# Kernel tuning notes

Hardware: AMD Instinct MI355X
Metric: run time of the kernel (lower is better)

The kernel has to match this reference:

```python
import jax, jax.numpy as jnp
import numpy as np

B, DIM, IN_DIM, H, W = 4, 256, 128, 128, 128
DD = IN_DIM // 2          # down_dim = 64
HEADS = 8
BN_EPS = 1e-5


def conv2d(x, w, b=None, pad=0, dil=1):
    y = jax.lax.conv_general_dilated(
        x, w, window_strides=(1, 1),
        padding=[(pad, pad), (pad, pad)],
        rhs_dilation=(dil, dil),
        dimension_numbers=('NCHW', 'OIHW', 'NCHW'))
    if b is not None:
        y = y + b[None, :, None, None]
    return y


def bn_relu(x, s, o):
    # eval-mode BatchNorm2d with running_mean=0, running_var=1
    return jax.nn.relu(x * (s / np.sqrt(1.0 + BN_EPS))[None, :, None, None] + o[None, :, None, None])


def setup_inputs() -> dict:
    ks = iter(jax.random.split(jax.random.key(0), 80))

    def w(shape, sc=0.05):
        return sc * jax.random.normal(next(ks), shape, jnp.float32)

    def s(c):
        return 1.0 + 0.1 * jax.random.normal(next(ks), (c,), jnp.float32)

    def o(c):
        return 0.02 * jax.random.normal(next(ks), (c,), jnp.float32)

    d = {}
    d['x'] = jax.random.normal(next(ks), (B, DIM, H, W), jnp.float32)
    d['w_dc'] = w((IN_DIM, DIM, 3, 3)); d['b_dc'] = w((IN_DIM,)); d['s_dc'] = s(IN_DIM); d['o_dc'] = o(IN_DIM)
    d['w1'] = w((DD, IN_DIM, 1, 1)); d['b1'] = w((DD,)); d['s1'] = s(DD); d['o1'] = o(DD)
    d['w2'] = w((DD, DD, 3, 3)); d['b2'] = w((DD,)); d['s2'] = s(DD); d['o2'] = o(DD)
    d['w3'] = w((DD, DD, 3, 3)); d['b3'] = w((DD,)); d['s3'] = s(DD); d['o3'] = o(DD)
    d['w4'] = w((DD, DD, 3, 3)); d['b4'] = w((DD,)); d['s4'] = s(DD); d['o4'] = o(DD)
    d['w5'] = w((DD, IN_DIM, 1, 1)); d['b5'] = w((DD,)); d['s5'] = s(DD); d['o5'] = o(DD)
    d['temperature'] = jnp.ones((HEADS, 1, 1), jnp.float32)
    d['w_po'] = w((DD, 2 * DD, 1, 1))  # project_out, bias=False
    d['w_wa'] = w((DD // 16, DD, 1, 1)); d['b_wa'] = w((DD // 16,)); d['s_wa'] = s(DD // 16); d['o_wa'] = o(DD // 16)
    d['w_wb'] = w((DD, DD // 16, 1, 1)); d['b_wb'] = w((DD,))
    d['w_f'] = w((DD, 5 * DD, 1, 1)); d['b_f'] = w((DD,)); d['s_f'] = s(DD); d['o_f'] = o(DD)
    d['w_oa'] = w((DD // 2, DD, 3, 3)); d['b_oa'] = w((DD // 2,)); d['s_oa'] = s(DD // 2); d['o_oa'] = o(DD // 2)
    d['w_ob'] = w((1, DD // 2, 1, 1)); d['b_ob'] = w((1,))
    return d


def reference(x, w_dc, b_dc, s_dc, o_dc, w1, b1, s1, o1, w2, b2, s2, o2,
              w3, b3, s3, o3, w4, b4, s4, o4, w5, b5, s5, o5,
              temperature, w_po, w_wa, b_wa, s_wa, o_wa, w_wb, b_wb,
              w_f, b_f, s_f, o_f, w_oa, b_oa, s_oa, o_oa, w_ob, b_ob):

    def branch(c):
        b, ch, h, wd = c.shape
        f = jnp.fft.fft2(c)                                   # [b,ch,h,w] complex64 (q=k=v=tepqkv)
        qkv = f.reshape(b, HEADS, ch // HEADS, h * wd)        # v (unnormalized)
        n = jnp.sqrt(jnp.sum(jnp.square(jnp.abs(qkv)), axis=-1, keepdims=True))
        qn = qkv / jnp.maximum(n, 1e-12)                      # F.normalize(dim=-1); q == k
        attn = jnp.einsum('bhcn,bhdn->bhcd', qn, qn) * temperature
        # custom complex normalization: separate real/imag softmax
        attn = jax.lax.complex(jax.nn.softmax(attn.real, axis=-1),
                               jax.nn.softmax(attn.imag, axis=-1))
        of = jnp.abs(jnp.fft.ifft2(jnp.einsum('bhcd,bhdn->bhcn', attn, qkv)))  # ifft2 over (c, hw)
        of = of.reshape(b, ch, h, wd)
        g = jax.nn.sigmoid(conv2d(bn_relu(conv2d(f.real, w_wa, b_wa), s_wa, o_wa), w_wb, b_wb))
        ol = jnp.abs(jnp.fft.ifft2(g * f))                    # ifft2 over (h, w)
        return conv2d(jnp.concatenate([of, ol], axis=1), w_po) + c

    xd = bn_relu(conv2d(x, w_dc, b_dc, pad=1), s_dc, o_dc)
    c1 = bn_relu(conv2d(xd, w1, b1), s1, o1)
    c2 = bn_relu(conv2d(c1, w2, b2, pad=3, dil=3), s2, o2)
    F2 = branch(c2)
    c3 = bn_relu(conv2d(c1 + F2, w3, b3, pad=5, dil=5), s3, o3)
    F3 = branch(c3)
    c4 = bn_relu(conv2d(c1 + F3, w4, b4, pad=7, dil=7), s4, o4)
    F4 = branch(c4)
    # conv5: global avg pool -> 1x1 conv -> bilinear upsample of a 1x1 map == broadcast
    c5 = bn_relu(conv2d(jnp.mean(xd, axis=(2, 3), keepdims=True), w5, b5), s5, o5)
    c5 = jnp.broadcast_to(c5, (c5.shape[0], c5.shape[1], xd.shape[2], xd.shape[3]))
    fused = bn_relu(conv2d(jnp.concatenate([c1, F2, F3, F4, c5], axis=1), w_f, b_f), s_f, o_f)
    return conv2d(bn_relu(conv2d(fused, w_oa, b_oa, pad=1), s_oa, o_oa), w_ob, b_ob)
```

## Files before the change

kernel.cpp:

```cpp
#include <hip/hip_runtime.h>

#define S 16384
#define PI_F 3.14159265358979f

struct Ptrs { const float* p[43]; };

enum : int {
  O_SBDC=0, O_SB1=256, O_SB2=512, O_SB3=768, O_SB4=1024, O_SB5=1280,
  O_SBWA=1536, O_SBF=1792, O_SBOA=2048,
  O_M=2304, O_C5=2816, O_NRM=3072, O_GRAM=3328, O_ATT2=7424, O_BEFF=11520,
  O_WB=16384,
  O_PART=147456,
  O_H=180224,
  O_WP=442368,
  O_A=524288,
  O_FIN=8912896,
  O_CC=25690112,
  O_DRE=29884416, O_DIMG=34078720,
  O_ERE=38273024, O_EIM=42467328,
  O_G=46661632
};

typedef short bfrag __attribute__((ext_vector_type(8)));
typedef float ffrag __attribute__((ext_vector_type(4)));

__device__ __forceinline__ float bf2f(unsigned short u){
  union { unsigned int i; float f; } v; v.i = ((unsigned int)u) << 16; return v.f;
}
__device__ __forceinline__ unsigned short f2bf(float f){
  unsigned int x = __float_as_uint(f);
  unsigned int r = x + 0x7fffu + ((x >> 16) & 1u);
  return (unsigned short)(r >> 16);
}

__global__ void prep_sb_kernel(Ptrs P, float* ws){
  const float r = rsqrtf(1.0f + 1e-5f);
  int bi=0, si=0, oi=0, C=0, dst=0;
  switch (blockIdx.x){
    case 0: bi=2; si=3; oi=4; C=128; dst=O_SBDC; break;
    case 1: bi=6; si=7; oi=8; C=64; dst=O_SB1; break;
    case 2: bi=10; si=11; oi=12; C=64; dst=O_SB2; break;
    case 3: bi=14; si=15; oi=16; C=64; dst=O_SB3; break;
    case 4: bi=18; si=19; oi=20; C=64; dst=O_SB4; break;
    case 5: bi=22; si=23; oi=24; C=64; dst=O_SB5; break;
    case 6: bi=28; si=29; oi=30; C=4;  dst=O_SBWA; break;
    case 7: bi=34; si=35; oi=36; C=64; dst=O_SBF; break;
    default: bi=38; si=39; oi=40; C=32; dst=O_SBOA; break;
  }
  for (int c = threadIdx.x; c < C; c += 256){
    float bb = P.p[bi][c], ss = P.p[si][c], oo = P.p[oi][c];
    float sc = ss * r;
    ws[dst + c] = sc;
    ws[dst + C + c] = bb * sc + oo;
  }
}

__global__ __launch_bounds__(256) void xpad_kernel(const float* __restrict__ x,
    unsigned short* __restrict__ XT){
  int yy = blockIdx.x, b = blockIdx.y;
  long obase = ((long)(b*130) + yy) * (130L*256);
  int tid = threadIdx.x;
  if (yy == 0 || yy == 129){
    uint4 z; z.x=0; z.y=0; z.z=0; z.w=0;
    for (int i = tid; i < 130*256/8; i += 256)
      *(uint4*)(XT + obase + (long)i*8) = z;
    return;
  }
  __shared__ float LT[64][129];
  int y = yy - 1;
  for (int c0 = 0; c0 < 256; c0 += 64){
    for (int idx = tid; idx < 64*128; idx += 256){
      int ci = idx >> 7, xx = idx & 127;
      LT[ci][xx] = x[((long)(b*256 + c0 + ci)*128 + y)*128 + xx];
    }
    __syncthreads();
    for (int idx = tid; idx < 128*16; idx += 256){
      int xp = idx >> 4, c4 = (idx & 15)*4;
      ushort4 v;
      v.x = f2bf(LT[c4][xp]);   v.y = f2bf(LT[c4+1][xp]);
      v.z = f2bf(LT[c4+2][xp]); v.w = f2bf(LT[c4+3][xp]);
      *(ushort4*)(XT + obase + (long)(xp+1)*256 + c0 + c4) = v;
    }
    __syncthreads();
  }
  if (tid < 64){
    ushort4 z; z.x=0; z.y=0; z.z=0; z.w=0;
    *(ushort4*)(XT + obase + tid*4) = z;
    *(ushort4*)(XT + obase + 129L*256 + tid*4) = z;
  }
}

__global__ void wt_kernel(const float* __restrict__ w, unsigned short* __restrict__ WH,
    unsigned short* __restrict__ WL){
  for (int e = blockIdx.x*256 + threadIdx.x; e < 294912; e += gridDim.x*256){
    int c32 = e & 31, co = (e >> 5) & 127, kc = (e >> 12) & 7, sh = e >> 15;
    int ky = sh / 3, kx = sh - ky*3;
    int ci = kc*32 + c32;
    float v = w[((long)(co*256 + ci)*3 + ky)*3 + kx];
    unsigned short h = f2bf(v);
    WH[e] = h;
    WL[e] = f2bf(v - bf2f(h));
  }
}

__global__ void wtg_kernel(Ptrs P, unsigned short* __restrict__ WB){
  const float* w; int cout; long off;
  switch (blockIdx.y){
    case 0: w = P.p[9];  cout = 64; off = 0;      break;
    case 1: w = P.p[13]; cout = 64; off = 73728;  break;
    case 2: w = P.p[17]; cout = 64; off = 147456; break;
    default: w = P.p[37]; cout = 32; off = 221184; break;
  }
  int total = 576*cout;
  unsigned short* WH = WB + off;
  unsigned short* WL = WH + total;
  for (int e = blockIdx.x*256 + threadIdx.x; e < total; e += gridDim.x*256){
    int c32 = e & 31;
    int co = (e >> 5) & (cout - 1);
    int kc = (e / (32*cout)) & 1;
    int sh = e / (64*cout);
    int ky = sh/3, kx = sh - ky*3;
    int ci = kc*32 + c32;
    float v = w[((long)(co*64 + ci)*3 + ky)*3 + kx];
    unsigned short h = f2bf(v);
    WH[e] = h;
    WL[e] = f2bf(v - bf2f(h));
  }
}

__global__ void wtp_kernel(Ptrs P, unsigned short* __restrict__ WP){
  const float* w; int KC, wstr; long off;
  switch (blockIdx.y){
    case 0: w = P.p[5];  KC = 4; wstr = 128; off = 0;     break;
    case 1: w = P.p[26]; KC = 4; wstr = 128; off = 16384; break;
    default: w = P.p[33]; KC = 8; wstr = 320; off = 32768; break;
  }
  int total = KC*64*32;
  unsigned short* WH = WP + off;
  unsigned short* WL = WH + total;
  for (int e = blockIdx.x*256 + threadIdx.x; e < total; e += gridDim.x*256){
    int c32 = e & 31, co = (e >> 5) & 63, kc = e >> 11;
    float v = w[(long)co*wstr + kc*32 + c32];
    unsigned short h = f2bf(v);
    WH[e] = h;
    WL[e] = f2bf(v - bf2f(h));
  }
}

template<int DIL>
__global__ __launch_bounds__(256) void xpad64_kernel(const float* __restrict__ in1,
    const float* __restrict__ in2, long in_bs, unsigned short* __restrict__ XP){
  constexpr int TW = 128 + 2*DIL;
  int yy = blockIdx.x, b = blockIdx.y;
  long obase = (long)(b*TW + yy) * TW * 64;
  int tid = threadIdx.x;
  if (yy < DIL || yy >= 128 + DIL){
    uint4 z; z.x=0; z.y=0; z.z=0; z.w=0;
    for (int i = tid; i < TW*8; i += 256)
      *(uint4*)(XP + obase + (long)i*8) = z;
    return;
  }
  __shared__ float LT[64][129];
  int y = yy - DIL;
  const float* p1 = in1 + (long)b*in_bs + (long)y*128;
  const float* p2 = in2 ? in2 + (long)b*in_bs + (long)y*128 : nullptr;
  for (int idx = tid; idx < 64*128; idx += 256){
    int ci = idx >> 7, xx = idx & 127;
    float v = p1[(long)ci*S + xx];
    if (p2) v += p2[(long)ci*S + xx];
    LT[ci][xx] = v;
  }
  __syncthreads();
  for (int i = tid; i < 2*DIL*16; i += 256){
    int side = i / (DIL*16);
    int r = i - side*(DIL*16);
    int xcol = side ? (128 + DIL + (r >> 4)) : (r >> 4);
    ushort4 z; z.x=0; z.y=0; z.z=0; z.w=0;
    *(ushort4*)(XP + obase + (long)xcol*64 + (r & 15)*4) = z;
  }
  for (int idx = tid; idx < 128*16; idx += 256){
    int xp = idx >> 4, c4 = (idx & 15)*4;
    ushort4 v;
    v.x = f2bf(LT[c4][xp]);   v.y = f2bf(LT[c4+1][xp]);
    v.z = f2bf(LT[c4+2][xp]); v.w = f2bf(LT[c4+3][xp]);
    *(ushort4*)(XP + obase + (long)(xp + DIL)*64 + c4) = v;
  }
}

template<int DIL, int KC, int NBLK>
__global__ __launch_bounds__(256) void conv3x3_mfma_kernel(
    const unsigned short* __restrict__ XP,
    const unsigned short* __restrict__ WH, const unsigned short* __restrict__ WL,
    const float* __restrict__ scbi, float* __restrict__ out){
  constexpr int CIN = KC*32;
  constexpr int TW = 128 + 2*DIL;
  constexpr int NJ = NBLK/32;
  constexpr int LDA = 36;
  constexpr int NSTG = (TW + 63)/64;
  constexpr int NS = 3*KC;
  __shared__ unsigned short As[2][TW*LDA];
  int bid = blockIdx.x;
  int y = (bid & 7)*16 + ((bid >> 3) & 15);
  int b = (bid >> 7) & 3;
  int n2 = bid >> 9;
  int nb = gridDim.x >> 9; if (nb == 0) nb = 1;
  int coutTotal = nb * NBLK;
  int tid = threadIdx.x, wv = tid >> 6, lane = tid & 63;
  int mhalf = wv & 1, nhalf = wv >> 1;
  int px0 = mhalf*64;
  ffrag acc[4][NJ];
  #pragma unroll
  for (int i = 0; i < 4; i++)
    #pragma unroll
    for (int j = 0; j < NJ; j++)
      #pragma unroll
      for (int r = 0; r < 4; r++) acc[i][j][r] = 0.f;

  int kq = (lane >> 4)*8, rown = lane & 15;
  int sx = tid >> 2, sq = tid & 3;
  int cobase = n2*NBLK + nhalf*(NBLK/2);

  {
    long rowbase = ((long)(b*TW + y))*TW*CIN + sq*8;
    #pragma unroll
    for (int t = 0; t < NSTG; t++){
      int x = sx + 64*t;
      int xc = x < TW ? x : TW - 1;
      uint4 v = *(const uint4*)(XP + rowbase + (long)xc*CIN);
      if (x < TW) *(uint4*)&As[0][x*LDA + sq*8] = v;
    }
  }
  __syncthreads();

  for (int s = 0; s < NS; s++){
    int cur = s & 1;
    int ky = s / KC, kc = s - ky*KC;
    int s2 = (s + 1 < NS) ? s + 1 : s;
    int ky2 = s2 / KC, kc2 = s2 - ky2*KC;
    uint4 pre[NSTG];
    {
      long rowbase = ((long)(b*TW + y + ky2*DIL))*TW*CIN + kc2*32 + sq*8;
      #pragma unroll
      for (int t = 0; t < NSTG; t++){
        int x = sx + 64*t;
        int xc = x < TW ? x : TW - 1;
        pre[t] = *(const uint4*)(XP + rowbase + (long)xc*CIN);
      }
    }
    #pragma unroll
    for (int kx = 0; kx < 3; kx++){
      int step = (ky*3 + kx)*KC + kc;
      bfrag bhf[NJ], blf[NJ];
      #pragma unroll
      for (int j = 0; j < NJ; j++){
        long wb = ((long)step*coutTotal + cobase + j*16 + rown)*32 + kq;
        bhf[j] = *(const bfrag*)(WH + wb);
        blf[j] = *(const bfrag*)(WL + wb);
      }
      bfrag af[4];
      #pragma unroll
      for (int i = 0; i < 4; i++){
        int x = px0 + i*16 + rown + kx*DIL;
        af[i] = *(const bfrag*)&As[cur][x*LDA + kq];
      }
      #pragma unroll
      for (int i = 0; i < 4; i++)
        #pragma unroll
        for (int j = 0; j < NJ; j++){
          acc[i][j] = __builtin_amdgcn_mfma_f32_16x16x32_bf16(af[i], blf[j], acc[i][j], 0, 0, 0);
          acc[i][j] = __builtin_amdgcn_mfma_f32_16x16x32_bf16(af[i], bhf[j], acc[i][j], 0, 0, 0);
        }
    }
    #pragma unroll
    for (int t = 0; t < NSTG; t++){
      int x = sx + 64*t;
      if (x < TW) *(uint4*)&As[cur ^ 1][x*LDA + sq*8] = pre[t];
    }
    __syncthreads();
  }
  #pragma unroll
  for (int i = 0; i < 4; i++){
    int pixel = px0 + i*16 + (lane >> 4)*4;
    #pragma unroll
    for (int j = 0; j < NJ; j++){
      int co = cobase + j*16 + (lane & 15);
      float sc = scbi[co], bb = scbi[coutTotal + co];
      float* op = out + ((long)(b*coutTotal + co))*S + y*128 + pixel;
      #pragma unroll
      for (int r = 0; r < 4; r++)
        op[r] = fmaxf(acc[i][j][r]*sc + bb, 0.f);
    }
  }
}

template<int MODE, int KC, int BF16IN>
__global__ __launch_bounds__(256) void conv1x1_mfma_kernel(
    const void* __restrict__ inv, long in_bs,
    const unsigned short* __restrict__ WH, const unsigned short* __restrict__ WL,
    const float* __restrict__ scbi, const float* __restrict__ beff,
    const float* __restrict__ res, long res_bs,
    float* __restrict__ out, long out_bs){
  constexpr int LDA = 36;
  __shared__ unsigned short Als[128*LDA];
  __shared__ unsigned short BHs[64*LDA];
  __shared__ unsigned short BLs[64*LDA];
  int bid = blockIdx.x;
  int y = (bid & 7)*16 + ((bid >> 3) & 15);
  int b = bid >> 7;
  int tid = threadIdx.x, wv = tid >> 6, lane = tid & 63;
  int mt0 = (wv & 1)*4, nt0 = (wv >> 1)*2;
  ffrag acc[4][2];
  #pragma unroll
  for (int i = 0; i < 4; i++)
    #pragma unroll
    for (int j = 0; j < 2; j++)
      #pragma unroll
      for (int r = 0; r < 4; r++) acc[i][j][r] = 0.f;
  int pq = tid & 31, cg = tid >> 5;
  int kq = (lane >> 4)*8, rown = lane & 15;
  int wrB = (tid >> 2)*LDA + (tid & 3)*8;
  const float* ibf = (const float*)inv + (long)b*in_bs + y*128;
  const unsigned short* ibs = (const unsigned short*)inv + (long)b*in_bs + y*128;
  unsigned short a[16];
  uint4 BHr, BLr;
  #pragma unroll
  for (int cc = 0; cc < 4; cc++)
    #pragma unroll
    for (int i = 0; i < 4; i++){
      if (BF16IN) a[cc*4 + i] = ibs[(long)(cg*4 + cc)*S + pq + 32*i];
      else        a[cc*4 + i] = f2bf(ibf[(long)(cg*4 + cc)*S + pq + 32*i]);
    }
  BHr = *(const uint4*)(WH + tid*8);
  BLr = *(const uint4*)(WL + tid*8);
  for (int kc = 0; kc < KC; kc++){
    __syncthreads();
    #pragma unroll
    for (int i = 0; i < 4; i++){
      ushort4 v;
      v.x = a[0 + i];  v.y = a[4 + i];
      v.z = a[8 + i];  v.w = a[12 + i];
      *(ushort4*)&Als[(pq + 32*i)*LDA + cg*4] = v;
    }
    *(uint4*)&BHs[wrB] = BHr;
    *(uint4*)&BLs[wrB] = BLr;
    __syncthreads();
    if (kc + 1 < KC){
      #pragma unroll
      for (int cc = 0; cc < 4; cc++)
        #pragma unroll
        for (int i = 0; i < 4; i++){
          long off = (long)((kc + 1)*32 + cg*4 + cc)*S + pq + 32*i;
          if (BF16IN) a[cc*4 + i] = ibs[off];
          else        a[cc*4 + i] = f2bf(ibf[off]);
        }
      long gw = (long)(kc + 1)*2048;
      BHr = *(const uint4*)(WH + gw + tid*8);
      BLr = *(const uint4*)(WL + gw + tid*8);
    }
    bfrag af[4], bhf[2], blf[2];
    #pragma unroll
    for (int i = 0; i < 4; i++)
      af[i] = *(const bfrag*)&Als[((mt0 + i)*16 + rown)*LDA + kq];
    #pragma unroll
    for (int j = 0; j < 2; j++){
      bhf[j] = *(const bfrag*)&BHs[((nt0 + j)*16 + rown)*LDA + kq];
      blf[j] = *(const bfrag*)&BLs[((nt0 + j)*16 + rown)*LDA + kq];
    }
    #pragma unroll
    for (int i = 0; i < 4; i++)
      #pragma unroll
      for (int j = 0; j < 2; j++){
        acc[i][j] = __builtin_amdgcn_mfma_f32_16x16x32_bf16(af[i], blf[j], acc[i][j], 0, 0, 0);
        acc[i][j] = __builtin_amdgcn_mfma_f32_16x16x32_bf16(af[i], bhf[j], acc[i][j], 0, 0, 0);
      }
  }
  #pragma unroll
  for (int i = 0; i < 4; i++){
    int pixel = (mt0 + i)*16 + (lane >> 4)*4;
    #pragma unroll
    for (int j = 0; j < 2; j++){
      int co = (nt0 + j)*16 + (lane & 15);
      float* op = out + (long)b*out_bs + (long)co*S + y*128 + pixel;
      #pragma unroll
      for (int r = 0; r < 4; r++){
        float v = acc[i][j][r];
        if (MODE == 0){
          v = fmaxf(v*scbi[co] + scbi[64 + co], 0.f);
        } else if (MODE == 1){
          v += res[(long)b*res_bs + (long)co*S + y*128 + pixel + r];
        } else {
          v = fmaxf(v*scbi[co] + beff[b*64 + co], 0.f);
        }
        op[r] = v;
      }
    }
  }
}

__device__ __forceinline__ void fft128_mk_tw(float (&tws)[8], float (&twc)[8],
                                             float sign, int lane){
  float a0 = sign * (2.0f*PI_F/128.0f) * (float)lane;
  __sincosf(a0, &tws[0], &twc[0]);
  int i = 1;
  #pragma unroll
  for (int h = 32; h >= 1; h >>= 1, i++){
    int j = lane & (h - 1);
    float a = sign * (2.0f*PI_F/128.0f) * (float)(j * (64/h));
    __sincosf(a, &tws[i], &twc[i]);
  }
}

__device__ __forceinline__ void fft128(float& z0r, float& z0i, float& z1r, float& z1i,
    const float (&tws)[8], const float (&twc)[8], int lane){
  {
    float ar = z0r, ai = z0i, br = z1r, bi = z1i;
    z0r = ar + br; z0i = ai + bi;
    float dr = ar - br, di = ai - bi;
    float s = tws[0], c = twc[0];
    z1r = dr*c - di*s; z1i = dr*s + di*c;
  }
  int idx = 1;
  #pragma unroll
  for (int h = 32; h >= 1; h >>= 1, idx++){
    float s = tws[idx], c = twc[idx];
    bool up = (lane & h) != 0;
    float pr, pi, nr, ni;
    pr = __shfl_xor(z0r, h, 64); pi = __shfl_xor(z0i, h, 64);
    if (!up){ nr = z0r + pr; ni = z0i + pi; }
    else { float dr = pr - z0r, di = pi - z0i; nr = dr*c - di*s; ni = dr*s + di*c; }
    z0r = nr; z0i = ni;
    pr = __shfl_xor(z1r, h, 64); pi = __shfl_xor(z1i, h, 64);
    if (!up){ nr = z1r + pr; ni = z1i + pi; }
    else { float dr = pr - z1r, di = pi - z1i; nr = dr*c - di*s; ni = dr*s + di*c; }
    z1r = nr; z1i = ni;
  }
}


__global__ __launch_bounds__(1024) void fft2_fwd_kernel(const float* __restrict__ in,
    unsigned short* __restrict__ outRe, unsigned short* __restrict__ outIm){
  __shared__ float lre[128][129];
  __shared__ float lim[128][129];
  int plane = blockIdx.x;
  int tid = threadIdx.x, wv = tid >> 6, lane = tid & 63;
  long pbase = (long)plane * S;
  for (int i = tid; i < S/4; i += 1024){
    int px = i*4; int r = px >> 7, c = px & 127;
    float4 v = *(const float4*)(in + pbase + px);
    lre[r][c] = v.x; lre[r][c+1] = v.y; lre[r][c+2] = v.z; lre[r][c+3] = v.w;
  }
  float tws[8], twc[8];
  fft128_mk_tw(tws, twc, -1.0f, lane);
  __syncthreads();
  #pragma unroll
  for (int rr = 0; rr < 8; rr++){
    int r = wv*8 + rr;
    float z0r = lre[r][lane], z0i = 0.f;
    float z1r = lre[r][lane + 64], z1i = 0.f;
    fft128(z0r, z0i, z1r, z1i, tws, twc, lane);
    int k = __brev(lane) >> 25;
    lre[r][k] = z0r;     lim[r][k] = z0i;
    lre[r][k+1] = z1r;   lim[r][k+1] = z1i;
  }
  __syncthreads();
  #pragma unroll
  for (int cc = 0; cc < 8; cc++){
    int c = wv*8 + cc;
    float z0r = lre[lane][c], z0i = lim[lane][c];
    float z1r = lre[lane + 64][c], z1i = lim[lane + 64][c];
    fft128(z0r, z0i, z1r, z1i, tws, twc, lane);
    int k = __brev(lane) >> 25;
    lre[k][c] = z0r;     lim[k][c] = z0i;
    lre[k+1][c] = z1r;   lim[k+1][c] = z1i;
  }
  __syncthreads();
  for (int i = tid; i < S/2; i += 1024){
    int px = i*2; int r = px >> 7, c = px & 127;
    ushort2 vr, vi;
    vr.x = f2bf(lre[r][c]); vr.y = f2bf(lre[r][c+1]);
    vi.x = f2bf(lim[r][c]); vi.y = f2bf(lim[r][c+1]);
    *(ushort2*)(outRe + pbase + px) = vr;
    *(ushort2*)(outIm + pbase + px) = vi;
  }
}

__global__ __launch_bounds__(1024) void ifft2_gate_abs_ol_kernel(
    const unsigned short* __restrict__ Dre, const unsigned short* __restrict__ Dim,
    const float* __restrict__ H, const float* __restrict__ wb, const float* __restrict__ bwb,
    unsigned short* __restrict__ AB){
  __shared__ float lre[128][129];
  __shared__ float lim[128][129];
  int plane = blockIdx.x;
  int b = plane >> 6, ch = plane & 63;
  int tid = threadIdx.x, wv = tid >> 6, lane = tid & 63;
  long pbase = (long)plane * S;
  float w0 = wb[ch*4], w1 = wb[ch*4+1], w2 = wb[ch*4+2], w3 = wb[ch*4+3];
  float bw = bwb[ch];
  const float* Hb = H + (long)b*4*S;
  for (int i = tid; i < S/2; i += 1024){
    int px = i*2;
    float2 h0 = *(const float2*)(Hb + px);
    float2 h1 = *(const float2*)(Hb + S + px);
    float2 h2 = *(const float2*)(Hb + 2*S + px);
    float2 h3 = *(const float2*)(Hb + 3*S + px);
    ushort2 ur = *(const ushort2*)(Dre + pbase + px);
    ushort2 ui = *(const ushort2*)(Dim + pbase + px);
    float hva = bw + w0*h0.x + w1*h1.x + w2*h2.x + w3*h3.x;
    float hvb = bw + w0*h0.y + w1*h1.y + w2*h2.y + w3*h3.y;
    float ga = 1.0f / (1.0f + __expf(-hva));
    float gb = 1.0f / (1.0f + __expf(-hvb));
    int r = px >> 7, c = px & 127;
    lre[r][c]   = bf2f(ur.x) * ga;  lim[r][c]   = bf2f(ui.x) * ga;
    lre[r][c+1] = bf2f(ur.y) * gb;  lim[r][c+1] = bf2f(ui.y) * gb;
  }
  float tws[8], twc[8];
  fft128_mk_tw(tws, twc, 1.0f, lane);
  __syncthreads();
  #pragma unroll
  for (int cc = 0; cc < 8; cc++){
    int c = wv*8 + cc;
    float z0r = lre[lane][c], z0i = lim[lane][c];
    float z1r = lre[lane + 64][c], z1i = lim[lane + 64][c];
    fft128(z0r, z0i, z1r, z1i, tws, twc, lane);
    int k = __brev(lane) >> 25;
    lre[k][c] = z0r;     lim[k][c] = z0i;
    lre[k+1][c] = z1r;   lim[k+1][c] = z1i;
  }
  __syncthreads();
  unsigned short* out = AB + ((long)(b*128 + 64 + ch)) * S;
  #pragma unroll
  for (int rr = 0; rr < 8; rr++){
    int r = wv*8 + rr;
    float z0r = lre[r][lane], z0i = lim[r][lane];
    float z1r = lre[r][lane + 64], z1i = lim[r][lane + 64];
    fft128(z0r, z0i, z1r, z1i, tws, twc, lane);
    int k = __brev(lane) >> 25;
    ushort2 v;
    v.x = f2bf(sqrtf(z0r*z0r + z0i*z0i) * (1.0f/16384.0f));
    v.y = f2bf(sqrtf(z1r*z1r + z1i*z1i) * (1.0f/16384.0f));
    *(ushort2*)(out + (long)r*128 + k) = v;
  }
}

__global__ __launch_bounds__(1024) void ifft2_attn_abs_ofT_kernel(
    const unsigned short* __restrict__ Dre, const unsigned short* __restrict__ Dim,
    const float* __restrict__ ATT2, unsigned short* __restrict__ AB){
  __shared__ float lre[128][129];
  __shared__ float lim[128][129];
  int plane = blockIdx.x;
  int b = plane >> 6, ch = plane & 63;
  int bh = plane >> 3;
  int cp = plane & 7;
  int tid = threadIdx.x, wv = tid >> 6, lane = tid & 63;
  long hbase = (long)bh * 8 * S;
  float wr[8], wi[8];
  #pragma unroll
  for (int d = 0; d < 8; d++){
    wr[d] = ATT2[bh*128 + (cp*8 + d)*2];
    wi[d] = ATT2[bh*128 + (cp*8 + d)*2 + 1];
  }
  for (int i = tid; i < S/4; i += 1024){
    int px = i*4;
    float sr0=0.f, si0=0.f, sr1=0.f, si1=0.f, sr2=0.f, si2=0.f, sr3=0.f, si3=0.f;
    #pragma unroll
    for (int d = 0; d < 8; d++){
      ushort4 ur = *(const ushort4*)(Dre + hbase + (long)d*S + px);
      ushort4 ui = *(const ushort4*)(Dim + hbase + (long)d*S + px);
      float xr0 = bf2f(ur.x), xi0 = bf2f(ui.x);
      float xr1 = bf2f(ur.y), xi1 = bf2f(ui.y);
      float xr2 = bf2f(ur.z), xi2 = bf2f(ui.z);
      float xr3 = bf2f(ur.w), xi3 = bf2f(ui.w);
      sr0 += wr[d]*xr0 - wi[d]*xi0;  si0 += wr[d]*xi0 + wi[d]*xr0;
      sr1 += wr[d]*xr1 - wi[d]*xi1;  si1 += wr[d]*xi1 + wi[d]*xr1;
      sr2 += wr[d]*xr2 - wi[d]*xi2;  si2 += wr[d]*xi2 + wi[d]*xr2;
      sr3 += wr[d]*xr3 - wi[d]*xi3;  si3 += wr[d]*xi3 + wi[d]*xr3;
    }
    int r = px >> 7, c = px & 127;
    lre[r][c]   = sr0;  lim[r][c]   = si0;
    lre[r][c+1] = sr1;  lim[r][c+1] = si1;
    lre[r][c+2] = sr2;  lim[r][c+2] = si2;
    lre[r][c+3] = sr3;  lim[r][c+3] = si3;
  }
  float tws[8], twc[8];
  fft128_mk_tw(tws, twc, 1.0f, lane);
  __syncthreads();
  #pragma unroll
  for (int cc = 0; cc < 8; cc++){
    int c = wv*8 + cc;
    float z0r = lre[lane][c], z0i = lim[lane][c];
    float z1r = lre[lane + 64][c], z1i = lim[lane + 64][c];
    fft128(z0r, z0i, z1r, z1i, tws, twc, lane);
    int k = __brev(lane) >> 25;
    float s, co;
    float a0 = (2.0f*PI_F/16384.0f) * (float)(c * k);
    __sincosf(a0, &s, &co);
    float t = z0r*co - z0i*s; z0i = z0r*s + z0i*co; z0r = t;
    float a1 = (2.0f*PI_F/16384.0f) * (float)(c * (k + 1));
    __sincosf(a1, &s, &co);
    t = z1r*co - z1i*s; z1i = z1r*s + z1i*co; z1r = t;
    lre[k][c] = z0r;     lim[k][c] = z0i;
    lre[k+1][c] = z1r;   lim[k+1][c] = z1i;
  }
  __syncthreads();
  float absv[8][2];
  #pragma unroll
  for (int rr = 0; rr < 8; rr++){
    int r = wv*8 + rr;
    float z0r = lre[r][lane], z0i = lim[r][lane];
    float z1r = lre[r][lane + 64], z1i = lim[r][lane + 64];
    fft128(z0r, z0i, z1r, z1i, tws, twc, lane);
    absv[rr][0] = sqrtf(z0r*z0r + z0i*z0i) * (1.0f/16384.0f);
    absv[rr][1] = sqrtf(z1r*z1r + z1i*z1i) * (1.0f/16384.0f);
  }
  __syncthreads();
  int k2 = __brev(lane) >> 25;
  #pragma unroll
  for (int rr = 0; rr < 8; rr++){
    int r = wv*8 + rr;
    lre[k2][r] = absv[rr][0];
    lre[k2+1][r] = absv[rr][1];
  }
  __syncthreads();
  unsigned short* out = AB + ((long)(b*128 + ch)) * S;
  for (int i = tid; i < S/2; i += 1024){
    int px = i*2; int r = px >> 7, c = px & 127;
    ushort2 v;
    v.x = f2bf(lre[r][c]); v.y = f2bf(lre[r][c+1]);
    *(ushort2*)(out + px) = v;
  }
}

__global__ __launch_bounds__(256) void gram_part_kernel(
    const unsigned short* __restrict__ Dre, const unsigned short* __restrict__ Dim,
    float* __restrict__ PART){
  int bh = blockIdx.x, slab = blockIdx.y;
  long base = (long)bh * 8 * S;
  int n0 = slab * 2048;
  float accr[36], acci[36], nsq[8];
  #pragma unroll
  for (int i = 0; i < 36; i++){ accr[i] = 0.f; acci[i] = 0.f; }
  #pragma unroll
  for (int i = 0; i < 8; i++) nsq[i] = 0.f;
  for (int it = 0; it < 4; it++){
    int n = n0 + (it*256 + threadIdx.x)*2;
    float xr[8][2], xi[8][2];
    #pragma unroll
    for (int c = 0; c < 8; c++){
      ushort2 ur = *(const ushort2*)(Dre + base + (long)c*S + n);
      ushort2 ui = *(const ushort2*)(Dim + base + (long)c*S + n);
      xr[c][0] = bf2f(ur.x); xr[c][1] = bf2f(ur.y);
      xi[c][0] = bf2f(ui.x); xi[c][1] = bf2f(ui.y);
      nsq[c] += xr[c][0]*xr[c][0] + xi[c][0]*xi[c][0]
              + xr[c][1]*xr[c][1] + xi[c][1]*xi[c][1];
    }
    int t = 0;
    #pragma unroll
    for (int c = 0; c < 8; c++)
      #pragma unroll
      for (int d = c; d < 8; d++){
        accr[t] += xr[c][0]*xr[d][0] - xi[c][0]*xi[d][0]
                 + xr[c][1]*xr[d][1] - xi[c][1]*xi[d][1];
        acci[t] += xr[c][0]*xi[d][0] + xi[c][0]*xr[d][0]
                 + xr[c][1]*xi[d][1] + xi[c][1]*xr[d][1];
        t++;
      }
  }
  __shared__ float red[4][80];
  int wv = threadIdx.x >> 6, lane = threadIdx.x & 63;
  #pragma unroll
  for (int i = 0; i < 80; i++){
    float v = (i < 36) ? accr[i] : (i < 72) ? acci[i - 36] : nsq[i - 72];
    #pragma unroll
    for (int o = 32; o; o >>= 1) v += __shfl_xor(v, o, 64);
    if (lane == 0) red[wv][i] = v;
  }
  __syncthreads();
  if (threadIdx.x < 80){
    int i = threadIdx.x;
    PART[(long)(bh*8 + slab)*80 + i] = red[0][i] + red[1][i] + red[2][i] + red[3][i];
  }
}

__global__ void attn2f_kernel(const float* __restrict__ PART,
    const float* __restrict__ temp, float* __restrict__ ATT2){
  __shared__ float ssum[80];
  __shared__ float sar[64], sai[64];
  int bh = blockIdx.x;
  int t = threadIdx.x;
  if (t < 80){
    float s = 0.f;
    for (int i = 0; i < 8; i++) s += PART[(long)(bh*8 + i)*80 + t];
    ssum[t] = s;
  }
  __syncthreads();
  if (t >= 64) return;
  int lane = t;
  int c = lane >> 3, d = lane & 7;
  int lo = min(c, d), hi = max(c, d);
  int t2 = lo*8 - lo*(lo - 1)/2 + (hi - lo);
  float nnc = fmaxf(sqrtf(ssum[72 + c]), 1e-12f);
  float nnd = fmaxf(sqrtf(ssum[72 + d]), 1e-12f);
  float inv = temp[bh & 7] / (nnc * nnd);
  float ar = ssum[t2] * inv, ai = ssum[36 + t2] * inv;
  float m = ar;
  m = fmaxf(m, __shfl_xor(m, 1, 64)); m = fmaxf(m, __shfl_xor(m, 2, 64)); m = fmaxf(m, __shfl_xor(m, 4, 64));
  float e = __expf(ar - m);
  float su = e;
  su += __shfl_xor(su, 1, 64); su += __shfl_xor(su, 2, 64); su += __shfl_xor(su, 4, 64);
  ar = e / su;
  m = ai;
  m = fmaxf(m, __shfl_xor(m, 1, 64)); m = fmaxf(m, __shfl_xor(m, 2, 64)); m = fmaxf(m, __shfl_xor(m, 4, 64));
  e = __expf(ai - m);
  su = e;
  su += __shfl_xor(su, 1, 64); su += __shfl_xor(su, 2, 64); su += __shfl_xor(su, 4, 64);
  ai = e / su;
  sar[lane] = ar; sai[lane] = ai;
  __syncthreads();
  const float ct[8] = {1.f, 0.70710678f, 0.f, -0.70710678f, -1.f, -0.70710678f, 0.f, 0.70710678f};
  const float st[8] = {0.f, 0.70710678f, 1.f, 0.70710678f, 0.f, -0.70710678f, -1.f, -0.70710678f};
  int cp = c;
  float sr = 0.f, si = 0.f;
  #pragma unroll
  for (int cc = 0; cc < 8; cc++){
    int k = (cc * cp) & 7;
    float a = sar[cc*8 + d], b2 = sai[cc*8 + d];
    sr += ct[k]*a - st[k]*b2;
    si += ct[k]*b2 + st[k]*a;
  }
  float2 v; v.x = sr * 0.125f; v.y = si * 0.125f;
  ((float2*)ATT2)[bh*64 + lane] = v;
}

__global__ __launch_bounds__(256) void gateh_kernel(const unsigned short* __restrict__ Dre,
    const float* __restrict__ wa, const float* __restrict__ sbwa, float* __restrict__ H){
  int b = blockIdx.y;
  int px = blockIdx.x*256 + threadIdx.x;
  long base = (long)b * 64 * S + px;
  float h0 = 0.f, h1 = 0.f, h2 = 0.f, h3 = 0.f;
  for (int ci = 0; ci < 64; ci++){
    float x = bf2f(Dre[base + (long)ci*S]);
    h0 += wa[ci]*x; h1 += wa[64 + ci]*x; h2 += wa[128 + ci]*x; h3 += wa[192 + ci]*x;
  }
  long ob = (long)b * 4 * S + px;
  H[ob]       = fmaxf(h0*sbwa[0] + sbwa[4], 0.f);
  H[ob + S]   = fmaxf(h1*sbwa[1] + sbwa[5], 0.f);
  H[ob + 2*S] = fmaxf(h2*sbwa[2] + sbwa[6], 0.f);
  H[ob + 3*S] = fmaxf(h3*sbwa[3] + sbwa[7], 0.f);
}

__global__ __launch_bounds__(256) void mean_kernel(const float* __restrict__ A, float* __restrict__ M){
  int p = blockIdx.x;
  long base = (long)p * S;
  float s = 0.f;
  for (int n = threadIdx.x; n < S; n += 256) s += A[base + n];
  #pragma unroll
  for (int o = 32; o; o >>= 1) s += __shfl_xor(s, o, 64);
  __shared__ float sm[4];
  if ((threadIdx.x & 63) == 0) sm[threadIdx.x >> 6] = s;
  __syncthreads();
  if (threadIdx.x == 0) M[p] = (sm[0] + sm[1] + sm[2] + sm[3]) * (1.0f/16384.0f);
}

__global__ void c5beff_kernel(const float* __restrict__ W5, const float* __restrict__ sb5,
    const float* __restrict__ WF, const float* __restrict__ sbf,
    const float* __restrict__ M, float* __restrict__ BEFF){
  __shared__ float c5s[256];
  int t = threadIdx.x;
  if (t >= 256) return;
  int b = t >> 6, co = t & 63;
  float s = 0.f;
  for (int ci = 0; ci < 128; ci++) s += W5[co*128 + ci] * M[b*128 + ci];
  c5s[t] = fmaxf(s * sb5[co] + sb5[64 + co], 0.f);
  __syncthreads();
  float s2 = 0.f;
  for (int j = 0; j < 64; j++) s2 += WF[co*320 + 256 + j] * c5s[b*64 + j];
  BEFF[t] = s2 * sbf[co] + sbf[64 + co];
}

__global__ __launch_bounds__(256) void ob_kernel(const float* __restrict__ Tin,
    const float* __restrict__ wob, const float* __restrict__ bob, float* __restrict__ out){
  int b = blockIdx.y;
  int px = blockIdx.x*1024 + (threadIdx.x & 63)*4 + (threadIdx.x >> 6)*256;
  float b0 = bob[0];
  float4 a; a.x = b0; a.y = b0; a.z = b0; a.w = b0;
  for (int ci = 0; ci < 32; ci++){
    float4 v = *(const float4*)(Tin + ((long)b*32 + ci)*S + px);
    float w = wob[ci];
    a.x += w*v.x; a.y += w*v.y; a.z += w*v.z; a.w += w*v.w;
  }
  *(float4*)(out + (long)b*S + px) = a;
}

extern "C" void kernel_launch(void* const* d_in, const int* in_sizes, int n_in,
                              void* d_out, int out_size, void* d_ws, size_t ws_size,
                              hipStream_t stream){
  float* ws = (float*)d_ws;
  Ptrs P;
  for (int i = 0; i < 43 && i < n_in; i++) P.p[i] = (const float*)d_in[i];
  float* out = (float*)d_out;

  float* A   = ws + O_A;
  float* FIN = ws + O_FIN;
  float* CC  = ws + O_CC;
  float* G   = ws + O_G;
  float* H   = ws + O_H;

  unsigned short* DRE16 = (unsigned short*)(ws + O_DRE);
  unsigned short* DIM16 = (unsigned short*)(ws + O_DIMG);
  unsigned short* AB    = (unsigned short*)(ws + O_A);

  unsigned short* XT  = (unsigned short*)(ws + O_DRE);
  unsigned short* WHd = (unsigned short*)(ws + O_CC);
  unsigned short* WLd = (unsigned short*)(ws + O_CC + 147456);
  unsigned short* WB  = (unsigned short*)(ws + O_WB);
  unsigned short* WP  = (unsigned short*)(ws + O_WP);
  unsigned short* XP  = (unsigned short*)(ws + O_ERE);

  prep_sb_kernel<<<dim3(9), dim3(256), 0, stream>>>(P, ws);
  xpad_kernel<<<dim3(130, 4), dim3(256), 0, stream>>>(P.p[0], XT);
  wt_kernel<<<dim3(128), dim3(256), 0, stream>>>(P.p[1], WHd, WLd);
  wtg_kernel<<<dim3(16, 4), dim3(256), 0, stream>>>(P, WB);
  wtp_kernel<<<dim3(8, 3), dim3(256), 0, stream>>>(P, WP);

  conv3x3_mfma_kernel<1,8,128><<<dim3(512), dim3(256), 0, stream>>>(
      XT, WHd, WLd, ws + O_SBDC, A);

  mean_kernel<<<dim3(512), dim3(256), 0, stream>>>(A, ws + O_M);
  c5beff_kernel<<<dim3(1), dim3(256), 0, stream>>>(
      P.p[21], ws + O_SB5, P.p[33], ws + O_SBF, ws + O_M, ws + O_BEFF);

  conv1x1_mfma_kernel<0,4,0><<<dim3(512), dim3(256), 0, stream>>>(
      A, 128*S, WP, WP + 8192, ws + O_SB1, nullptr, nullptr, 0, FIN, 256*S);

  for (int k = 0; k < 3; k++){
    const float* sb = ws + (k == 0 ? O_SB2 : k == 1 ? O_SB3 : O_SB4);
    const float* in2 = (k == 0) ? nullptr : FIN + (long)(64*k)*S;
    unsigned short* wh = WB + (k == 0 ? 0 : k == 1 ? 73728 : 147456);
    if (k == 0){
      xpad64_kernel<3><<<dim3(134, 4), dim3(256), 0, stream>>>(FIN, in2, 256*S, XP);
      conv3x3_mfma_kernel<3,2,64><<<dim3(512), dim3(256), 0, stream>>>(
          XP, wh, wh + 36864, sb, CC);
    } else if (k == 1){
      xpad64_kernel<5><<<dim3(138, 4), dim3(256), 0, stream>>>(FIN, in2, 256*S, XP);
      conv3x3_mfma_kernel<5,2,64><<<dim3(512), dim3(256), 0, stream>>>(
          XP, wh, wh + 36864, sb, CC);
    } else {
      xpad64_kernel<7><<<dim3(142, 4), dim3(256), 0, stream>>>(FIN, in2, 256*S, XP);
      conv3x3_mfma_kernel<7,2,64><<<dim3(512), dim3(256), 0, stream>>>(
          XP, wh, wh + 36864, sb, CC);
    }

    fft2_fwd_kernel<<<dim3(256), dim3(1024), 0, stream>>>(CC, DRE16, DIM16);
    gram_part_kernel<<<dim3(32, 8), dim3(256), 0, stream>>>(DRE16, DIM16, ws + O_PART);
    attn2f_kernel<<<dim3(32), dim3(128), 0, stream>>>(ws + O_PART, P.p[25], ws + O_ATT2);
    gateh_kernel<<<dim3(64, 4), dim3(256), 0, stream>>>(DRE16, P.p[27], ws + O_SBWA, H);
    ifft2_gate_abs_ol_kernel<<<dim3(256), dim3(1024), 0, stream>>>(
        DRE16, DIM16, H, P.p[31], P.p[32], AB);
    ifft2_attn_abs_ofT_kernel<<<dim3(256), dim3(1024), 0, stream>>>(
        DRE16, DIM16, ws + O_ATT2, AB);
    conv1x1_mfma_kernel<1,4,1><<<dim3(512), dim3(256), 0, stream>>>(
        AB, 128*S, WP + 16384, WP + 24576, nullptr, nullptr, CC, 64*S,
        FIN + (long)(64*(k + 1))*S, 256*S);
  }

  conv1x1_mfma_kernel<2,8,0><<<dim3(512), dim3(256), 0, stream>>>(
      FIN, 256*S, WP + 32768, WP + 49152, ws + O_SBF, ws + O_BEFF, nullptr, 0, CC, 64*S);
  xpad64_kernel<1><<<dim3(130, 4), dim3(256), 0, stream>>>(CC, nullptr, 64*S, XP);
  conv3x3_mfma_kernel<1,2,32><<<dim3(512), dim3(256), 0, stream>>>(
      XP, WB + 221184, WB + 221184 + 18432, ws + O_SBOA, G);
  ob_kernel<<<dim3(16, 4), dim3(256), 0, stream>>>(G, P.p[41], P.p[42], out);
}
```

Before: 924.6 us.

## Store intermediate feature maps FIN and CC in bf16 instead of fp32

Intermediate activations (the FIN concat buffer and the CC conv output) are now written and read as bf16 across the dilated conv, FFT input, 1x1 projection residual and fusion conv. This halves memory traffic for those buffers and uses vectorized ushort4 stores. The first 3x3 conv is also relaunched with a 64-wide cout block and a grid twice as large. The cost is reduced precision on values that were previously kept in fp32, such as the residual add inputs.

```diff
diff --git a/kernel.cpp b/kernel.cpp
--- a/kernel.cpp
+++ b/kernel.cpp
@@ -147,9 +147,9 @@
   }
 }
 
-template<int DIL>
-__global__ __launch_bounds__(256) void xpad64_kernel(const float* __restrict__ in1,
-    const float* __restrict__ in2, long in_bs, unsigned short* __restrict__ XP){
+template<int DIL, int BF16IN>
+__global__ __launch_bounds__(256) void xpad64_kernel(const void* __restrict__ in1,
+    const void* __restrict__ in2, long in_bs, unsigned short* __restrict__ XP){
   constexpr int TW = 128 + 2*DIL;
   int yy = blockIdx.x, b = blockIdx.y;
   long obase = (long)(b*TW + yy) * TW * 64;
@@ -162,13 +162,25 @@
   }
   __shared__ float LT[64][129];
   int y = yy - DIL;
-  const float* p1 = in1 + (long)b*in_bs + (long)y*128;
-  const float* p2 = in2 ? in2 + (long)b*in_bs + (long)y*128 : nullptr;
-  for (int idx = tid; idx < 64*128; idx += 256){
-    int ci = idx >> 7, xx = idx & 127;
-    float v = p1[(long)ci*S + xx];
-    if (p2) v += p2[(long)ci*S + xx];
-    LT[ci][xx] = v;
+  if (BF16IN){
+    const unsigned short* p1 = (const unsigned short*)in1 + (long)b*in_bs + (long)y*128;
+    const unsigned short* p2 = in2 ? (const unsigned short*)in2 + (long)b*in_bs + (long)y*128 : nullptr;
+    for (int idx = tid; idx < 64*64; idx += 256){
+      int ci = idx >> 6, x2 = (idx & 63)*2;
+      ushort2 u1 = *(const ushort2*)(p1 + (long)ci*S + x2);
+      float a0 = bf2f(u1.x), a1 = bf2f(u1.y);
+      if (p2){
+        ushort2 u2 = *(const ushort2*)(p2 + (long)ci*S + x2);
+        a0 += bf2f(u2.x); a1 += bf2f(u2.y);
+      }
+      LT[ci][x2] = a0; LT[ci][x2+1] = a1;
+    }
+  } else {
+    const float* p1 = (const float*)in1 + (long)b*in_bs + (long)y*128;
+    for (int idx = tid; idx < 64*128; idx += 256){
+      int ci = idx >> 7, xx = idx & 127;
+      LT[ci][xx] = p1[(long)ci*S + xx];
+    }
   }
   __syncthreads();
   for (int i = tid; i < 2*DIL*16; i += 256){
@@ -187,11 +199,11 @@
   }
 }
 
-template<int DIL, int KC, int NBLK>
+template<int DIL, int KC, int NBLK, int BF16OUT>
 __global__ __launch_bounds__(256) void conv3x3_mfma_kernel(
     const unsigned short* __restrict__ XP,
     const unsigned short* __restrict__ WH, const unsigned short* __restrict__ WL,
-    const float* __restrict__ scbi, float* __restrict__ out){
+    const float* __restrict__ scbi, void* __restrict__ out){
   constexpr int CIN = KC*32;
   constexpr int TW = 128 + 2*DIL;
   constexpr int NJ = NBLK/32;
@@ -285,21 +297,31 @@
     for (int j = 0; j < NJ; j++){
       int co = cobase + j*16 + (lane & 15);
       float sc = scbi[co], bb = scbi[coutTotal + co];
-      float* op = out + ((long)(b*coutTotal + co))*S + y*128 + pixel;
-      #pragma unroll
-      for (int r = 0; r < 4; r++)
-        op[r] = fmaxf(acc[i][j][r]*sc + bb, 0.f);
-    }
-  }
-}
-
-template<int MODE, int KC, int BF16IN>
+      long ooff = ((long)(b*coutTotal + co))*S + y*128 + pixel;
+      if (BF16OUT){
+        ushort4 w;
+        w.x = f2bf(fmaxf(acc[i][j][0]*sc + bb, 0.f));
+        w.y = f2bf(fmaxf(acc[i][j][1]*sc + bb, 0.f));
+        w.z = f2bf(fmaxf(acc[i][j][2]*sc + bb, 0.f));
+        w.w = f2bf(fmaxf(acc[i][j][3]*sc + bb, 0.f));
+        *(ushort4*)((unsigned short*)out + ooff) = w;
+      } else {
+        float* op = (float*)out + ooff;
+        #pragma unroll
+        for (int r = 0; r < 4; r++)
+          op[r] = fmaxf(acc[i][j][r]*sc + bb, 0.f);
+      }
+    }
+  }
+}
+
+template<int MODE, int KC, int BF16IN, int BF16OUT>
 __global__ __launch_bounds__(256) void conv1x1_mfma_kernel(
     const void* __restrict__ inv, long in_bs,
     const unsigned short* __restrict__ WH, const unsigned short* __restrict__ WL,
     const float* __restrict__ scbi, const float* __restrict__ beff,
-    const float* __restrict__ res, long res_bs,
-    float* __restrict__ out, long out_bs){
+    const unsigned short* __restrict__ res, long res_bs,
+    void* __restrict__ outv, long out_bs){
   constexpr int LDA = 36;
   __shared__ unsigned short Als[128*LDA];
   __shared__ unsigned short BHs[64*LDA];
@@ -380,18 +402,31 @@
     #pragma unroll
     for (int j = 0; j < 2; j++){
       int co = (nt0 + j)*16 + (lane & 15);
-      float* op = out + (long)b*out_bs + (long)co*S + y*128 + pixel;
-      #pragma unroll
-      for (int r = 0; r < 4; r++){
-        float v = acc[i][j][r];
-        if (MODE == 0){
-          v = fmaxf(v*scbi[co] + scbi[64 + co], 0.f);
-        } else if (MODE == 1){
-          v += res[(long)b*res_bs + (long)co*S + y*128 + pixel + r];
-        } else {
-          v = fmaxf(v*scbi[co] + beff[b*64 + co], 0.f);
-        }
-        op[r] = v;
+      long ooff = (long)b*out_bs + (long)co*S + y*128 + pixel;
+      float vv[4];
+      if (MODE == 1){
+        ushort4 rv = *(const ushort4*)(res + (long)b*res_bs + (long)co*S + y*128 + pixel);
+        vv[0] = acc[i][j][0] + bf2f(rv.x);
+        vv[1] = acc[i][j][1] + bf2f(rv.y);
+        vv[2] = acc[i][j][2] + bf2f(rv.z);
+        vv[3] = acc[i][j][3] + bf2f(rv.w);
+      } else if (MODE == 0){
+        #pragma unroll
+        for (int r = 0; r < 4; r++)
+          vv[r] = fmaxf(acc[i][j][r]*scbi[co] + scbi[64 + co], 0.f);
+      } else {
+        #pragma unroll
+        for (int r = 0; r < 4; r++)
+          vv[r] = fmaxf(acc[i][j][r]*scbi[co] + beff[b*64 + co], 0.f);
+      }
+      if (BF16OUT){
+        ushort4 w;
+        w.x = f2bf(vv[0]); w.y = f2bf(vv[1]); w.z = f2bf(vv[2]); w.w = f2bf(vv[3]);
+        *(ushort4*)((unsigned short*)outv + ooff) = w;
+      } else {
+        float* op = (float*)outv + ooff;
+        #pragma unroll
+        for (int r = 0; r < 4; r++) op[r] = vv[r];
       }
     }
   }
@@ -437,7 +472,7 @@
 }
 
 
-__global__ __launch_bounds__(1024) void fft2_fwd_kernel(const float* __restrict__ in,
+__global__ __launch_bounds__(1024) void fft2_fwd_kernel(const unsigned short* __restrict__ in,
     unsigned short* __restrict__ outRe, unsigned short* __restrict__ outIm){
   __shared__ float lre[128][129];
   __shared__ float lim[128][129];
@@ -446,8 +481,9 @@
   long pbase = (long)plane * S;
   for (int i = tid; i < S/4; i += 1024){
     int px = i*4; int r = px >> 7, c = px & 127;
-    float4 v = *(const float4*)(in + pbase + px);
-    lre[r][c] = v.x; lre[r][c+1] = v.y; lre[r][c+2] = v.z; lre[r][c+3] = v.w;
+    ushort4 v = *(const ushort4*)(in + pbase + px);
+    lre[r][c] = bf2f(v.x); lre[r][c+1] = bf2f(v.y);
+    lre[r][c+2] = bf2f(v.z); lre[r][c+3] = bf2f(v.w);
   }
   float tws[8], twc[8];
   fft128_mk_tw(tws, twc, -1.0f, lane);
@@ -800,11 +836,12 @@
   float* out = (float*)d_out;
 
   float* A   = ws + O_A;
-  float* FIN = ws + O_FIN;
   float* CC  = ws + O_CC;
   float* G   = ws + O_G;
   float* H   = ws + O_H;
 
+  unsigned short* FINB = (unsigned short*)(ws + O_FIN);
+  unsigned short* CCB  = (unsigned short*)(ws + O_CC);
   unsigned short* DRE16 = (unsigned short*)(ws + O_DRE);
   unsigned short* DIM16 = (unsigned short*)(ws + O_DIMG);
   unsigned short* AB    = (unsigned short*)(ws + O_A);
@@ -822,35 +859,35 @@
   wtg_kernel<<<dim3(16, 4), dim3(256), 0, stream>>>(P, WB);
   wtp_kernel<<<dim3(8, 3), dim3(256), 0, stream>>>(P, WP);
 
-  conv3x3_mfma_kernel<1,8,128><<<dim3(512), dim3(256), 0, stream>>>(
+  conv3x3_mfma_kernel<1,8,64,0><<<dim3(1024), dim3(256), 0, stream>>>(
       XT, WHd, WLd, ws + O_SBDC, A);
 
   mean_kernel<<<dim3(512), dim3(256), 0, stream>>>(A, ws + O_M);
   c5beff_kernel<<<dim3(1), dim3(256), 0, stream>>>(
       P.p[21], ws + O_SB5, P.p[33], ws + O_SBF, ws + O_M, ws + O_BEFF);
 
-  conv1x1_mfma_kernel<0,4,0><<<dim3(512), dim3(256), 0, stream>>>(
-      A, 128*S, WP, WP + 8192, ws + O_SB1, nullptr, nullptr, 0, FIN, 256*S);
+  conv1x1_mfma_kernel<0,4,0,1><<<dim3(512), dim3(256), 0, stream>>>(
+      A, 128*S, WP, WP + 8192, ws + O_SB1, nullptr, nullptr, 0, FINB, 256*S);
 
   for (int k = 0; k < 3; k++){
     const float* sb = ws + (k == 0 ? O_SB2 : k == 1 ? O_SB3 : O_SB4);
-    const float* in2 = (k == 0) ? nullptr : FIN + (long)(64*k)*S;
+    const unsigned short* in2 = (k == 0) ? nullptr : FINB + (long)(64*k)*S;
     unsigned short* wh = WB + (k == 0 ? 0 : k == 1 ? 73728 : 147456);
     if (k == 0){
-      xpad64_kernel<3><<<dim3(134, 4), dim3(256), 0, stream>>>(FIN, in2, 256*S, XP);
-      conv3x3_mfma_kernel<3,2,64><<<dim3(512), dim3(256), 0, stream>>>(
-          XP, wh, wh + 36864, sb, CC);
+      xpad64_kernel<3,1><<<dim3(134, 4), dim3(256), 0, stream>>>(FINB, in2, 256*S, XP);
+      conv3x3_mfma_kernel<3,2,64,1><<<dim3(512), dim3(256), 0, stream>>>(
+          XP, wh, wh + 36864, sb, CCB);
     } else if (k == 1){
-      xpad64_kernel<5><<<dim3(138, 4), dim3(256), 0, stream>>>(FIN, in2, 256*S, XP);
-      conv3x3_mfma_kernel<5,2,64><<<dim3(512), dim3(256), 0, stream>>>(
-          XP, wh, wh + 36864, sb, CC);
+      xpad64_kernel<5,1><<<dim3(138, 4), dim3(256), 0, stream>>>(FINB, in2, 256*S, XP);
+      conv3x3_mfma_kernel<5,2,64,1><<<dim3(512), dim3(256), 0, stream>>>(
+          XP, wh, wh + 36864, sb, CCB);
     } else {
-      xpad64_kernel<7><<<dim3(142, 4), dim3(256), 0, stream>>>(FIN, in2, 256*S, XP);
-      conv3x3_mfma_kernel<7,2,64><<<dim3(512), dim3(256), 0, stream>>>(
-          XP, wh, wh + 36864, sb, CC);
-    }
-
-    fft2_fwd_kernel<<<dim3(256), dim3(1024), 0, stream>>>(CC, DRE16, DIM16);
+      xpad64_kernel<7,1><<<dim3(142, 4), dim3(256), 0, stream>>>(FINB, in2, 256*S, XP);
+      conv3x3_mfma_kernel<7,2,64,1><<<dim3(512), dim3(256), 0, stream>>>(
+          XP, wh, wh + 36864, sb, CCB);
+    }
+
+    fft2_fwd_kernel<<<dim3(256), dim3(1024), 0, stream>>>(CCB, DRE16, DIM16);
     gram_part_kernel<<<dim3(32, 8), dim3(256), 0, stream>>>(DRE16, DIM16, ws + O_PART);
     attn2f_kernel<<<dim3(32), dim3(128), 0, stream>>>(ws + O_PART, P.p[25], ws + O_ATT2);
     gateh_kernel<<<dim3(64, 4), dim3(256), 0, stream>>>(DRE16, P.p[27], ws + O_SBWA, H);
@@ -858,15 +895,15 @@
         DRE16, DIM16, H, P.p[31], P.p[32], AB);
     ifft2_attn_abs_ofT_kernel<<<dim3(256), dim3(1024), 0, stream>>>(
         DRE16, DIM16, ws + O_ATT2, AB);
-    conv1x1_mfma_kernel<1,4,1><<<dim3(512), dim3(256), 0, stream>>>(
-        AB, 128*S, WP + 16384, WP + 24576, nullptr, nullptr, CC, 64*S,
-        FIN + (long)(64*(k + 1))*S, 256*S);
-  }
-
-  conv1x1_mfma_kernel<2,8,0><<<dim3(512), dim3(256), 0, stream>>>(
-      FIN, 256*S, WP + 32768, WP + 49152, ws + O_SBF, ws + O_BEFF, nullptr, 0, CC, 64*S);
-  xpad64_kernel<1><<<dim3(130, 4), dim3(256), 0, stream>>>(CC, nullptr, 64*S, XP);
-  conv3x3_mfma_kernel<1,2,32><<<dim3(512), dim3(256), 0, stream>>>(
+    conv1x1_mfma_kernel<1,4,1,1><<<dim3(512), dim3(256), 0, stream>>>(
+        AB, 128*S, WP + 16384, WP + 24576, nullptr, nullptr, CCB, 64*S,
+        FINB + (long)(64*(k + 1))*S, 256*S);
+  }
+
+  conv1x1_mfma_kernel<2,8,1,0><<<dim3(512), dim3(256), 0, stream>>>(
+      FINB, 256*S, WP + 32768, WP + 49152, ws + O_SBF, ws + O_BEFF, nullptr, 0, CC, 64*S);
+  xpad64_kernel<1,0><<<dim3(130, 4), dim3(256), 0, stream>>>(CC, nullptr, 64*S, XP);
+  conv3x3_mfma_kernel<1,2,32,0><<<dim3(512), dim3(256), 0, stream>>>(
       XP, WB + 221184, WB + 221184 + 18432, ws + O_SBOA, G);
   ob_kernel<<<dim3(16, 4), dim3(256), 0, stream>>>(G, P.p[41], P.p[42], out);
 }
```

After: 895.1 us. 1.03x faster.
